# Optimization experiments

Measured on AMD Instinct MI355X. Metric: run time of the kernel, lower is better.

## Reference

```python
import jax, jax.numpy as jnp
import numpy as np

K_NN = 3
EPS = 1e-8
MASK_THRESH = 0.5


def _three_nn_interpolate(pts, known, feats):
    """pts: (B,N,3), known: (B,M,3), feats: (B,M,C) -> (B,N,C).
    Squared-distance 3-NN + inverse-distance weighted interpolation
    (pointnet2 three_nn / three_interpolate semantics)."""
    # (B,N,M) squared euclidean distances
    d2 = (jnp.sum(pts * pts, -1)[:, :, None]
          + jnp.sum(known * known, -1)[:, None, :]
          - 2.0 * jnp.einsum('bnd,bmd->bnm', pts, known))
    neg_d, idx = jax.lax.top_k(-d2, K_NN)          # (B,N,3)
    dist = jnp.maximum(-neg_d, 0.0)                # squared dists, clamp fp error
    dist_recip = 1.0 / (dist + EPS)
    weight = dist_recip / jnp.sum(dist_recip, -1, keepdims=True)  # (B,N,3)
    b_idx = jnp.arange(pts.shape[0])[:, None, None]
    gathered = feats[b_idx, idx]                   # (B,N,3,C)
    return jnp.sum(weight[..., None] * gathered, axis=2)  # (B,N,C)


def setup_inputs() -> dict:
    key = jax.random.key(0)
    ks = jax.random.split(key, 10)
    B, N, C = 4, 8192, 32
    M2, M3, M4, Mm = 8192, 4096, 2048, 4096
    sc = 10.0  # spread coords over a realistic metric range
    return {
        'points_mean': jax.random.normal(ks[0], (B, N, 3)) * sc,
        'known2': jax.random.normal(ks[1], (B, M2, 3)) * sc,
        'feats2': jax.random.normal(ks[2], (B, M2, C)),
        'known3': jax.random.normal(ks[3], (B, M3, 3)) * sc,
        'feats3': jax.random.normal(ks[4], (B, M3, C)),
        'known4': jax.random.normal(ks[5], (B, M4, 3)) * sc,
        'feats4': jax.random.normal(ks[6], (B, M4, C)),
        'match_points': jax.random.normal(ks[7], (B, Mm, 3)) * sc,
        'w_fc': jax.random.normal(ks[8], (64, 96)) * 0.1,
        'w_cls': jax.random.normal(ks[9], (1, 64)) * 0.1,
    }


def reference(points_mean, known2, feats2, known3, feats3, known4, feats4,
              match_points, w_fc, w_cls):
    p0 = _three_nn_interpolate(points_mean, known2, feats2)  # (B,N,32)
    p1 = _three_nn_interpolate(points_mean, known3, feats3)
    p2 = _three_nn_interpolate(points_mean, known4, feats4)
    pointwise = jnp.concatenate([p0, p1, p2], axis=-1) @ w_fc.T  # (B,N,64)
    pred_hm = pointwise @ w_cls.T                                 # (B,N,1)
    # GT mask: min distance to match points < 0.5 m
    d2 = (jnp.sum(points_mean * points_mean, -1)[:, :, None]
          + jnp.sum(match_points * match_points, -1)[:, None, :]
          - 2.0 * jnp.einsum('bnd,bmd->bnm', points_mean, match_points))
    min_d = jnp.sqrt(jnp.maximum(jnp.min(d2, axis=-1), 0.0))      # (B,N)
    gt_hm = (min_d < MASK_THRESH).astype(jnp.float32)
    return pred_hm, gt_hm
```

## Files before the change

### kernel.cpp

```cpp
#include <hip/hip_runtime.h>

typedef unsigned int u32;
typedef unsigned long long u64;
typedef float f32x2 __attribute__((ext_vector_type(2)));

#define NB 4
#define NQ 8192
#define MARGIN 0.0625f
#define NBKT 4096

#define OFF_C0   0u
#define OFF_C1   524288u
#define OFF_C2   786432u
#define OFF_CMP  917504u
#define OFF_SKEY 1179648u
#define OFF_BOX  2031616u
#define WS_NEW2  2068480u
#define OFF_CM   917504u
#define WS_OLD   (512u*1024 + 256u*1024 + 128u*1024 + 512u*1024)

struct __align__(32) CP { f32x2 x, y, z, w; };
struct DM { double x, y, z, w; };

__device__ __forceinline__ f32x2 fma2(f32x2 a, f32x2 b, f32x2 c) {
  return __builtin_elementwise_fma(a, b, c);
}

__device__ __forceinline__ void lexins(double& e0d, double& e1d, double& e2d,
                                       int& e0i, int& e1i, int& e2i,
                                       double d, int i) {
  if (d < e2d || (d == e2d && i < e2i)) {
    if (d < e0d || (d == e0d && i < e0i)) {
      e2d = e1d; e2i = e1i; e1d = e0d; e1i = e0i; e0d = d; e0i = i;
    } else if (d < e1d || (d == e1d && i < e1i)) {
      e2d = e1d; e2i = e1i; e1d = d; e1i = i;
    } else {
      e2d = d; e2i = i;
    }
  }
}

__device__ __forceinline__ void ins4(float kv, u32 idx,
                                     float& k0, float& k1, float& k2, float& k3,
                                     u32& i0, u32& i1, u32& i2, u32& i3) {
  if (kv < k3) {
    bool lt0 = kv < k0, lt1 = kv < k1, lt2 = kv < k2;
    k3 = lt2 ? k2 : kv;               i3 = lt2 ? i2 : idx;
    k2 = lt2 ? (lt1 ? k1 : kv) : k2;  i2 = lt2 ? (lt1 ? i1 : idx) : i2;
    k1 = lt1 ? (lt0 ? k0 : kv) : k1;  i1 = lt1 ? (lt0 ? i0 : idx) : i1;
    k0 = lt0 ? kv : k0;               i0 = lt0 ? idx : i0;
  }
}

__device__ __forceinline__ u32 spread10(u32 v) {
  v &= 0x3FFu;
  v = (v | (v << 16)) & 0x030000FFu;
  v = (v | (v << 8))  & 0x0300F00Fu;
  v = (v | (v << 4))  & 0x030C30C3u;
  v = (v | (v << 2))  & 0x09249249u;
  return v;
}
__device__ __forceinline__ u32 morton30(float x, float y, float z) {
  int xi = (int)((x + 64.f) * 8.f);
  int yi = (int)((y + 64.f) * 8.f);
  int zi = (int)((z + 64.f) * 8.f);
  xi = min(max(xi, 0), 1023); yi = min(max(yi, 0), 1023); zi = min(max(zi, 0), 1023);
  return spread10((u32)xi) | (spread10((u32)yi) << 1) | (spread10((u32)zi) << 2);
}

__device__ __forceinline__ size_t skey_abase(int arr) {
  return (arr == 0) ? 0 : (arr == 1) ? 32768 : (arr == 2) ? 49152
        : (arr == 3) ? 57344 : 73728;
}

__global__ __launch_bounds__(1024) void prep_csort(
    const float* __restrict__ k2p, const float* __restrict__ k3p,
    const float* __restrict__ k4p, const float* __restrict__ mmp,
    const float* __restrict__ pts, u64* __restrict__ skey) {
  __shared__ u32 hist[NBKT];
  const int arr = blockIdx.x, b = blockIdx.y, tid = threadIdx.x;
  const float* src = (arr == 0) ? k2p : (arr == 1) ? k3p : (arr == 2) ? k4p
                      : (arr == 3) ? mmp : pts;
  const int n = (arr == 0) ? 8192 : (arr == 1) ? 4096 : (arr == 2) ? 2048
                 : (arr == 3) ? 4096 : 8192;
  const float* sb = src + (size_t)b * n * 3;
  u64* skb = skey + skey_abase(arr) + (size_t)b * n;

  for (int i = tid; i < NBKT; i += 1024) hist[i] = 0;
  __syncthreads();
  for (int i = tid; i < n; i += 1024) {
    u32 k = morton30(sb[3 * i], sb[3 * i + 1], sb[3 * i + 2]);
    atomicAdd(&hist[k >> 18], 1u);
  }
  __syncthreads();
  for (int d = 1; d < NBKT; d <<= 1) {
    for (int i = tid; i < NBKT / (2 * d); i += 1024) {
      int idx = (2 * i + 2) * d - 1;
      hist[idx] += hist[idx - d];
    }
    __syncthreads();
  }
  if (tid == 0) hist[NBKT - 1] = 0;
  __syncthreads();
  for (int d = NBKT >> 1; d >= 1; d >>= 1) {
    for (int i = tid; i < NBKT / (2 * d); i += 1024) {
      int idx = (2 * i + 2) * d - 1;
      u32 t = hist[idx - d];
      hist[idx - d] = hist[idx];
      hist[idx] += t;
    }
    __syncthreads();
  }
  for (int i = tid; i < n; i += 1024) {
    u32 k = morton30(sb[3 * i], sb[3 * i + 1], sb[3 * i + 2]);
    u32 pos = atomicAdd(&hist[k >> 18], 1u);
    skb[pos] = ((u64)k << 32) | (u32)i;
  }
}

__global__ __launch_bounds__(512) void refine_emit(
    const float* __restrict__ k2p, const float* __restrict__ k3p,
    const float* __restrict__ k4p, const float* __restrict__ mmp,
    const float* __restrict__ pts, u64* __restrict__ skey,
    CP* __restrict__ c0, CP* __restrict__ c1, CP* __restrict__ c2,
    CP* __restrict__ cmp, float* __restrict__ boxes) {
  __shared__ u64 ex[512];
  const int widx = blockIdx.x, b = blockIdx.y, tid = threadIdx.x;
  int arr, win;
  if (widx < 16)      { arr = 0; win = widx; }
  else if (widx < 24) { arr = 1; win = widx - 16; }
  else if (widx < 28) { arr = 2; win = widx - 24; }
  else if (widx < 36) { arr = 3; win = widx - 28; }
  else                { arr = 4; win = widx - 36; }
  const float* src = (arr == 0) ? k2p : (arr == 1) ? k3p : (arr == 2) ? k4p
                      : (arr == 3) ? mmp : pts;
  const int n = (arr == 0) ? 8192 : (arr == 1) ? 4096 : (arr == 2) ? 2048
                 : (arr == 3) ? 4096 : 8192;
  u64* skb = skey + skey_abase(arr) + (size_t)b * n;
  const int e = win * 512 + tid;
  u64 v = skb[e];

  for (int k = 2; k <= 512; k <<= 1) {
    for (int j = k >> 1; j > 0; j >>= 1) {
      u64 w;
      if (j < 64) {
        w = __shfl_xor(v, j);
      } else {
        __syncthreads();
        ex[tid] = v;
        __syncthreads();
        w = ex[tid ^ j];
      }
      bool up = (tid & k) == 0;
      bool lower = (tid & j) == 0;
      v = (up == lower) ? (v < w ? v : w) : (v < w ? w : v);
    }
  }
  skb[e] = v;
  if (arr == 4) return;

  u32 p = (u32)v;
  const float* sb = src + (size_t)b * n * 3;
  float x = sb[3 * p], y = sb[3 * p + 1], z = sb[3 * p + 2];
  {
    CP* dst = (arr == 0) ? c0 : (arr == 1) ? c1 : (arr == 2) ? c2 : cmp;
    float* df = (float*)(dst + (size_t)b * (n >> 1) + (e >> 1));
    int sl = e & 1;
    df[sl]     = x;
    df[2 + sl] = y;
    df[4 + sl] = z;
    df[6 + sl] = fmaf(z, z, fmaf(y, y, x * x));
  }
  float xlo = x, xhi = x, ylo = y, yhi = y, zlo = z, zhi = z;
#pragma unroll
  for (int off = 1; off < 64; off <<= 1) {
    xlo = fminf(xlo, __shfl_xor(xlo, off)); xhi = fmaxf(xhi, __shfl_xor(xhi, off));
    ylo = fminf(ylo, __shfl_xor(ylo, off)); yhi = fmaxf(yhi, __shfl_xor(yhi, off));
    zlo = fminf(zlo, __shfl_xor(zlo, off)); zhi = fmaxf(zhi, __shfl_xor(zhi, off));
  }
  if ((tid & 63) == 0) {
    const int nG = n >> 6, g = e >> 6;
    const int boff = (arr == 0) ? 0 : (arr == 1) ? 512 : (arr == 2) ? 768 : 896;
    float* bx = boxes + ((size_t)boff + (size_t)b * nG + g) * 8;
    bx[0] = xlo; bx[1] = xhi; bx[2] = ylo; bx[3] = yhi; bx[4] = zlo; bx[5] = zhi;
    bx[6] = 0.f; bx[7] = 0.f;
  }
}

__device__ __forceinline__ void scan_pairs16(
    const CP* __restrict__ cg, u32 ebase,
    f32x2 mx2, f32x2 my2, f32x2 mz2,
    float& k0, float& k1, float& k2, float& k3,
    u32& i0, u32& i1, u32& i2, u32& i3) {
#pragma unroll 4
  for (int gg = 0; gg < 16; gg += 4) {
    f32x2 key[4];
#pragma unroll
    for (int u = 0; u < 4; ++u) {
      CP c = cg[gg + u];
      key[u] = fma2(mx2, c.x, fma2(my2, c.y, fma2(mz2, c.z, c.w)));
    }
#pragma unroll
    for (int u = 0; u < 4; ++u) {
      float ka = key[u].x, kb = key[u].y;
      if (fminf(ka, kb) < k3) {
        u32 ib = ebase + (u32)((gg + u) * 2);
        ins4(ka, ib,     k0, k1, k2, k3, i0, i1, i2, i3);
        ins4(kb, ib + 1, k0, k1, k2, k3, i0, i1, i2, i3);
      }
    }
  }
}

struct Smem4 {
  float  box[2304];
  float  qx[32], qy[32], qz[32];
  double qdx[32], qdy[32], qdz[32], qn[32];
  u32    oq[32];
  u32    di[3][32][4][4];
  double mmin[32][8];
  float  wv[96];
  float  wq[32][9];
  u32    iq[32][9];
  float  contrib[32][9];
  float4 stage[4][2][64];
  u32    list[4][64];
};

__global__ __launch_bounds__(256, 4) void fused_sorted3(
    const float* __restrict__ pts,
    const float* __restrict__ f2, const float* __restrict__ f3,
    const float* __restrict__ f4,
    const float* __restrict__ wfc, const float* __restrict__ wcls,
    const CP* __restrict__ c0, const CP* __restrict__ c1,
    const CP* __restrict__ c2, const CP* __restrict__ cmp,
    const u64* __restrict__ skey, const float* __restrict__ boxes,
    float* __restrict__ out) {
  __shared__ Smem4 s;
  const int tid = threadIdx.x;
  const int b = blockIdx.y;
  const int tile = blockIdx.x;
  const int lane = tid & 63;
  const int q = tid & 31;
  const int h = (tid >> 5) & 1;
  const int wid = __builtin_amdgcn_readfirstlane(tid >> 6);

  for (int i = tid; i < 2304; i += 256) {
    int src;
    if (i < 1024)      src = (b * 128) * 8 + i;
    else if (i < 1536) src = (512 + b * 64) * 8 + (i - 1024);
    else if (i < 1792) src = (768 + b * 32) * 8 + (i - 1536);
    else               src = (896 + b * 64) * 8 + (i - 1792);
    s.box[i] = boxes[src];
  }
  if (tid < 32) {
    u64 kv = skey[73728 + (size_t)b * NQ + tile * 32 + tid];
    u32 p = (u32)kv;
    const float* pb = pts + (size_t)b * NQ * 3;
    float x = pb[3 * p], y = pb[3 * p + 1], z = pb[3 * p + 2];
    s.qx[tid] = x; s.qy[tid] = y; s.qz[tid] = z; s.oq[tid] = p;
    double dx = (double)x, dy = (double)y, dz = (double)z;
    s.qdx[tid] = dx; s.qdy[tid] = dy; s.qdz[tid] = dz;
    s.qn[tid] = (dx * dx + dy * dy) + dz * dz;
  } else if (tid < 128) {
    int t = tid - 32;
    float acc = 0.f;
    for (int j = 0; j < 64; ++j) acc += wcls[j] * wfc[j * 96 + t];
    s.wv[t] = acc;
  }
  __syncthreads();

  const float qx = s.qx[q], qy = s.qy[q], qz = s.qz[q];
  const float qnf = fmaf(qz, qz, fmaf(qy, qy, qx * qx));
  const float fm2x = -2.0f * qx, fm2y = -2.0f * qy, fm2z = -2.0f * qz;
  const double qdx = s.qdx[q], qdy = s.qdy[q], qdz = s.qdz[q], qn = s.qn[q];
  const f32x2 mx2 = {fm2x, fm2x}, my2 = {fm2y, fm2y}, mz2 = {fm2z, fm2z};

  {
    int lvl, part, nG, g0, stride, nvote, lboff;
    if (wid < 2)      { lvl = 0; nG = 128; stride = 2; nvote = 63;
                        g0 = (((tile * 128) >> 8) & ~1) | wid;
                        part = wid * 2 + h; lboff = 0; }
    else if (wid == 2){ lvl = 1; nG = 64;  stride = 1; nvote = 63;
                        g0 = (tile * 64) >> 8; part = h; lboff = 128; }
    else              { lvl = 2; nG = 32;  stride = 1; nvote = 31;
                        g0 = (tile * 32) >> 8; part = h; lboff = 192; }
    const int M = 8192 >> lvl;
    const CP* c4 = ((lvl == 0) ? c0 : ((lvl == 1) ? c1 : c2)) + (((size_t)b * M) >> 1);

    float k0 = __builtin_inff(), k1 = k0, k2 = k0, k3 = k0;
    u32 i0 = 0, i1 = 0, i2 = 0, i3 = 0;

    scan_pairs16(c4 + g0 * 32 + h * 16, (u32)(g0 * 64 + h * 32),
                 mx2, my2, mz2, k0, k1, k2, k3, i0, i1, i2, i3);

    int nl = 0;
    for (int t = 1; t <= nvote; ++t) {
      int g = (g0 + stride * t) & (nG - 1);
      const float* bx = &s.box[(lboff + g) * 8];
      float dx = fmaxf(fmaxf(bx[0] - qx, qx - bx[1]), 0.f);
      float dy = fmaxf(fmaxf(bx[2] - qy, qy - bx[3]), 0.f);
      float dz = fmaxf(fmaxf(bx[4] - qz, qz - bx[5]), 0.f);
      float lb = fmaf(dx, dx, fmaf(dy, dy, dz * dz));
      if (__any(lb < qnf + k3 + MARGIN)) {
        if (lane == 0) s.list[wid][nl] = (u32)g;
        ++nl;
      }
    }

    auto accept = [&](int g) -> bool {
      const float* bx = &s.box[(lboff + g) * 8];
      float dx = fmaxf(fmaxf(bx[0] - qx, qx - bx[1]), 0.f);
      float dy = fmaxf(fmaxf(bx[2] - qy, qy - bx[3]), 0.f);
      float dz = fmaxf(fmaxf(bx[4] - qz, qz - bx[5]), 0.f);
      float lb = fmaf(dx, dx, fmaf(dy, dy, dz * dz));
      return __any(lb < qnf + k3 + MARGIN);
    };
    int ip = 0, cur = 0, gcur = -1;
    float4 v;
    while (ip < nl) {
      int g = (int)s.list[wid][ip++];
      if (accept(g)) { gcur = g; v = ((const float4*)(c4 + (size_t)g * 32))[lane]; break; }
    }
    while (gcur >= 0) {
      s.stage[wid][cur][lane] = v;
      int gn = -1;
      while (ip < nl) {
        int g = (int)s.list[wid][ip++];
        if (accept(g)) { gn = g; break; }
      }
      if (gn >= 0) v = ((const float4*)(c4 + (size_t)gn * 32))[lane];
      const CP* sg = (const CP*)&s.stage[wid][cur][0];
      scan_pairs16(sg + h * 16, (u32)(gcur * 64 + h * 32),
                   mx2, my2, mz2, k0, k1, k2, k3, i0, i1, i2, i3);
      gcur = gn; cur ^= 1;
    }

    s.di[lvl][q][part][0] = i0; s.di[lvl][q][part][1] = i1;
    s.di[lvl][q][part][2] = i2; s.di[lvl][q][part][3] = i3;
  }

  {
    const CP* cmb = cmp + (size_t)b * 2048;
    int gm0 = tile >> 2;
    double dmin = __builtin_inf();
    for (int t = 0; t < 16; ++t) {
      int g = (gm0 + wid + 4 * t) & 63;
      const float* bx = &s.box[(224 + g) * 8];
      float dx = fmaxf(fmaxf(bx[0] - qx, qx - bx[1]), 0.f);
      float dy = fmaxf(fmaxf(bx[2] - qy, qy - bx[3]), 0.f);
      float dz = fmaxf(fmaxf(bx[4] - qz, qz - bx[5]), 0.f);
      float lb = fmaf(dx, dx, fmaf(dy, dy, dz * dz));
      if (__any(lb < 0.26f)) {
        const CP* cg = cmb + g * 32 + h * 16;
#pragma unroll 4
        for (int p = 0; p < 16; ++p) {
          CP c = cg[p];
          f32x2 key = fma2(mx2, c.x, fma2(my2, c.y, fma2(mz2, c.z, c.w)));
          if (fminf(key.x, key.y) + qnf < 0.252f) {
            {
              double x = (double)c.x.x, y = (double)c.y.x, z = (double)c.z.x;
              double kn2 = (x * x + y * y) + z * z;
              double dot = (qdx * x + qdy * y) + qdz * z;
              dmin = fmin(dmin, (qn + kn2) - 2.0 * dot);
            }
            {
              double x = (double)c.x.y, y = (double)c.y.y, z = (double)c.z.y;
              double kn2 = (x * x + y * y) + z * z;
              double dot = (qdx * x + qdy * y) + qdz * z;
              dmin = fmin(dmin, (qn + kn2) - 2.0 * dot);
            }
          }
        }
      }
    }
    s.mmin[q][wid * 2 + h] = dmin;
  }
  __syncthreads();

  const int gqbase = b * NQ;
  if (tid < 96) {
    const int lvl = tid >> 5;
    const int qq = tid & 31;
    const int M  = 8192 >> lvl;
    const int np = (lvl == 0) ? 4 : 2;
    const CP* c4 = ((lvl == 0) ? c0 : ((lvl == 1) ? c1 : c2)) + (((size_t)b * M) >> 1);
    const u64* skl = skey + ((lvl == 0) ? 0 : (lvl == 1) ? 32768 : 49152)
                     + (size_t)b * M;
    const double tqdx = s.qdx[qq], tqdy = s.qdy[qq], tqdz = s.qdz[qq], tqn = s.qn[qq];
    double e0 = __builtin_inf(), e1 = e0, e2 = e0;
    int j0 = 0, j1 = 0, j2 = 0;
    for (int hh = 0; hh < np; ++hh) {
#pragma unroll
      for (int r = 0; r < 4; ++r) {
        int sidx = (int)s.di[lvl][qq][hh][r];
        CP cc = c4[sidx >> 1];
        bool hi = sidx & 1;
        double x = (double)(hi ? cc.x.y : cc.x.x);
        double y = (double)(hi ? cc.y.y : cc.y.x);
        double z = (double)(hi ? cc.z.y : cc.z.x);
        int orig = (int)(u32)skl[sidx];
        double kn2 = (x * x + y * y) + z * z;
        double dot = (tqdx * x + tqdy * y) + tqdz * z;
        double d2 = (tqn + kn2) - 2.0 * dot;
        lexins(e0, e1, e2, j0, j1, j2, d2, orig);
      }
    }
    double d0 = fmax(e0, 0.0), d1 = fmax(e1, 0.0), d2v = fmax(e2, 0.0);
    double r0 = 1.0 / (d0 + 1e-8);
    double r1 = 1.0 / (d1 + 1e-8);
    double r2 = 1.0 / (d2v + 1e-8);
    double sum = (r0 + r1) + r2;
    s.wq[qq][lvl * 3 + 0] = (float)(r0 / sum); s.iq[qq][lvl * 3 + 0] = (u32)j0;
    s.wq[qq][lvl * 3 + 1] = (float)(r1 / sum); s.iq[qq][lvl * 3 + 1] = (u32)j1;
    s.wq[qq][lvl * 3 + 2] = (float)(r2 / sum); s.iq[qq][lvl * 3 + 2] = (u32)j2;
  } else if (tid < 128) {
    const int qq = tid - 96;
    double dm = s.mmin[qq][0];
#pragma unroll
    for (int p = 1; p < 8; ++p) dm = fmin(dm, s.mmin[qq][p]);
    out[NB * NQ + gqbase + (int)s.oq[qq]] = (dm < 0.25) ? 1.0f : 0.0f;
  }
  __syncthreads();

  for (int item = tid; item < 288; item += 256) {
    const int qq = item & 31, j = item >> 5;
    const int lvl = j / 3;
    const float* fp = (lvl == 0) ? f2 : ((lvl == 1) ? f3 : f4);
    const int M = 8192 >> lvl;
    const float4* row = (const float4*)(fp + ((size_t)b * M + s.iq[qq][j]) * 32);
    const float* wvp = s.wv + lvl * 32;
    float acc = 0.f;
#pragma unroll
    for (int v = 0; v < 8; ++v) {
      float4 r = row[v];
      acc += wvp[4 * v] * r.x + wvp[4 * v + 1] * r.y
           + wvp[4 * v + 2] * r.z + wvp[4 * v + 3] * r.w;
    }
    s.contrib[qq][j] = s.wq[qq][j] * acc;
  }
  __syncthreads();
  if (tid < 32) {
    const float* c = s.contrib[tid];
    float l0 = (c[0] + c[1]) + c[2];
    float l1 = (c[3] + c[4]) + c[5];
    float l2 = (c[6] + c[7]) + c[8];
    out[gqbase + (int)s.oq[tid]] = (l0 + l1) + l2;
  }
}

__global__ __launch_bounds__(256) void prep_kernel(
    const float* __restrict__ k2p, const float* __restrict__ k3p,
    const float* __restrict__ k4p, const float* __restrict__ mmp,
    CP* __restrict__ c0, CP* __restrict__ c1,
    CP* __restrict__ c2, DM* __restrict__ cm) {
  int r = blockIdx.y;
  int i = blockIdx.x * 256 + threadIdx.x;
  if (r < 3) {
    const float* src = (r == 0) ? k2p : ((r == 1) ? k3p : k4p);
    CP* dst = (r == 0) ? c0 : ((r == 1) ? c1 : c2);
    int pairs = (r == 0) ? NB * 4096 : ((r == 1) ? NB * 2048 : NB * 1024);
    if (i >= pairs) return;
    const float* p = src + (size_t)i * 6;
    float x0 = p[0], y0 = p[1], z0 = p[2];
    float x1 = p[3], y1 = p[4], z1 = p[5];
    CP c;
    c.x = f32x2{x0, x1}; c.y = f32x2{y0, y1}; c.z = f32x2{z0, z1};
    c.w = f32x2{fmaf(z0, z0, fmaf(y0, y0, x0 * x0)),
                fmaf(z1, z1, fmaf(y1, y1, x1 * x1))};
    dst[i] = c;
  } else {
    if (i >= NB * 4096) return;
    double x = (double)mmp[3 * i], y = (double)mmp[3 * i + 1], z = (double)mmp[3 * i + 2];
    DM d = {x, y, z, fma(z, z, fma(y, y, x * x))};
    cm[i] = d;
  }
}

template <bool PREP>
__device__ __forceinline__ void scan_nn(
    const CP* __restrict__ cp, const float* __restrict__ raw,
    int gstart, int L, float m2x, float m2y, float m2z,
    float* kk, u32* ii) {
  float k0 = __builtin_inff(), k1 = k0, k2 = k0, k3 = k0;
  u32 i0 = 0, i1 = 0, i2 = 0, i3 = 0;
  if (PREP) {
    const f32x2 mx2 = {m2x, m2x}, my2 = {m2y, m2y}, mz2 = {m2z, m2z};
    const int G = L >> 1;
#pragma unroll 2
    for (int g = 0; g < G; g += 4) {
      f32x2 key[4];
#pragma unroll
      for (int u = 0; u < 4; ++u) {
        CP c = cp[g + u];
        key[u] = fma2(mx2, c.x, fma2(my2, c.y, fma2(mz2, c.z, c.w)));
      }
#pragma unroll
      for (int u = 0; u < 4; ++u) {
        float ka = key[u].x, kb = key[u].y;
        if (fminf(ka, kb) < k3) {
          u32 ib = (u32)(gstart + 2 * (g + u));
          ins4(ka, ib,     k0, k1, k2, k3, i0, i1, i2, i3);
          ins4(kb, ib + 1, k0, k1, k2, k3, i0, i1, i2, i3);
        }
      }
    }
  } else {
    for (int j = 0; j < L; j += 8) {
      float key[8];
#pragma unroll
      for (int u = 0; u < 8; ++u) {
        const float* p = raw + (size_t)(gstart + j + u) * 3;
        float x = p[0], y = p[1], z = p[2];
        float n2 = fmaf(z, z, fmaf(y, y, x * x));
        key[u] = fmaf(m2x, x, fmaf(m2y, y, fmaf(m2z, z, n2)));
      }
#pragma unroll
      for (int u = 0; u < 8; ++u)
        ins4(key[u], (u32)(gstart + j + u), k0, k1, k2, k3, i0, i1, i2, i3);
    }
  }
  kk[0] = k0; kk[1] = k1; kk[2] = k2; kk[3] = k3;
  ii[0] = i0; ii[1] = i1; ii[2] = i2; ii[3] = i3;
}

template <bool PREP>
__device__ __forceinline__ double scan_mask(
    const DM* __restrict__ c8, const float* __restrict__ raw,
    int gstart, int L, double m2x, double m2y, double m2z) {
  double smin = __builtin_inf();
  if (PREP) {
    for (int j = 0; j < L; j += 8) {
      double sv[8];
#pragma unroll
      for (int u = 0; u < 8; ++u) {
        DM c = c8[gstart + j + u];
        sv[u] = fma(m2x, c.x, fma(m2y, c.y, fma(m2z, c.z, c.w)));
      }
      double m01 = fmin(sv[0], sv[1]), m23 = fmin(sv[2], sv[3]);
      double m45 = fmin(sv[4], sv[5]), m67 = fmin(sv[6], sv[7]);
      smin = fmin(smin, fmin(fmin(m01, m23), fmin(m45, m67)));
    }
  } else {
    for (int j = 0; j < L; j += 4) {
#pragma unroll
      for (int u = 0; u < 4; ++u) {
        const float* p = raw + (size_t)(gstart + j + u) * 3;
        double x = (double)p[0], y = (double)p[1], z = (double)p[2];
        double kn = fma(z, z, fma(y, y, x * x));
        smin = fmin(smin, fma(m2x, x, fma(m2y, y, fma(m2z, z, kn))));
      }
    }
  }
  return smin;
}

struct Smem {
  float  qx[64], qy[64], qz[64];
  double qdx[64], qdy[64], qdz[64], qn[64];
  float  dk[3][64][4][4];
  u32    di[3][64][4][4];
  double mmin[64][8];
  float  wv[96];
  float  part[64][3];
};

template <bool PREP>
__global__ __launch_bounds__(512, 2) void fused_kernel(
    const float* __restrict__ pts,
    const float* __restrict__ k2p, const float* __restrict__ f2,
    const float* __restrict__ k3p, const float* __restrict__ f3,
    const float* __restrict__ k4p, const float* __restrict__ f4,
    const float* __restrict__ mmp,
    const float* __restrict__ wfc, const float* __restrict__ wcls,
    const CP* __restrict__ c0, const CP* __restrict__ c1,
    const CP* __restrict__ c2, const DM* __restrict__ cm,
    float* __restrict__ out) {
  __shared__ Smem s;
  const int tid = threadIdx.x;
  const int b = blockIdx.y;
  const int q0 = blockIdx.x * 64;
  const int qloc = tid & 63;
  const int wid = __builtin_amdgcn_readfirstlane(tid >> 6);

  if (tid < 64) {
    int gq = b * NQ + q0 + tid;
    float x = pts[3 * gq], y = pts[3 * gq + 1], z = pts[3 * gq + 2];
    s.qx[tid] = x; s.qy[tid] = y; s.qz[tid] = z;
    double dx = (double)x, dy = (double)y, dz = (double)z;
    s.qdx[tid] = dx; s.qdy[tid] = dy; s.qdz[tid] = dz;
    s.qn[tid] = (dx * dx + dy * dy) + dz * dz;
  } else if (tid < 160) {
    int t = tid - 64;
    float acc = 0.f;
    for (int j = 0; j < 64; ++j) acc += wcls[j] * wfc[j * 96 + t];
    s.wv[t] = acc;
  }
  __syncthreads();

  const float fm2x = -2.0f * s.qx[qloc];
  const float fm2y = -2.0f * s.qy[qloc];
  const float fm2z = -2.0f * s.qz[qloc];
  const double dm2x = -2.0 * s.qdx[qloc];
  const double dm2y = -2.0 * s.qdy[qloc];
  const double dm2z = -2.0 * s.qdz[qloc];

  {
    int lvl, prt, gstart, glen;
    if (wid < 4)      { lvl = 0; prt = wid;     gstart = wid * 2048;       glen = 2048; }
    else if (wid < 6) { lvl = 1; prt = wid - 4; gstart = (wid - 4) * 2048; glen = 2048; }
    else              { lvl = 2; prt = wid - 6; gstart = (wid - 6) * 1024; glen = 1024; }
    const CP* c4 = (lvl == 0) ? c0 : ((lvl == 1) ? c1 : c2);
    const float* raw = (lvl == 0) ? k2p : ((lvl == 1) ? k3p : k4p);
    const int      M = (lvl == 0) ? 8192 : ((lvl == 1) ? 4096 : 2048);
    float kk[4]; u32 ii[4];
    scan_nn<PREP>(c4 + (PREP ? (((size_t)b * M + gstart) >> 1) : 0),
                  raw + (size_t)b * M * 3,
                  gstart, glen, fm2x, fm2y, fm2z, kk, ii);
#pragma unroll
    for (int r = 0; r < 4; ++r) {
      s.dk[lvl][qloc][prt][r] = kk[r];
      s.di[lvl][qloc][prt][r] = ii[r];
    }
    int mstart, mlen;
    if (wid < 6) { mstart = wid * 256; mlen = 256; }
    else         { mstart = 1536 + (wid - 6) * 1280; mlen = 1280; }
    s.mmin[qloc][wid] = scan_mask<PREP>(cm + (PREP ? (size_t)b * 4096 : 0),
                                        mmp + (size_t)b * 4096 * 3,
                                        mstart, mlen, dm2x, dm2y, dm2z);
  }
  __syncthreads();

  const int gqbase = b * NQ + q0;
  if (tid < 192) {
    const int lvl = __builtin_amdgcn_readfirstlane(tid >> 6);
    const int q = tid & 63;
    const float* kp = (lvl == 0) ? k2p : ((lvl == 1) ? k3p : k4p);
    const int    M  = (lvl == 0) ? 8192 : ((lvl == 1) ? 4096 : 2048);
    const int    np = (lvl == 0) ? 4 : 2;
    const double qdx = s.qdx[q], qdy = s.qdy[q], qdz = s.qdz[q], qn = s.qn[q];
    double e0 = __builtin_inf(), e1 = e0, e2 = e0;
    int i0 = 0, i1 = 0, i2 = 0;
    for (int h = 0; h < np; ++h) {
#pragma unroll
      for (int r = 0; r < 4; ++r) {
        int idx = (int)s.di[lvl][q][h][r];
        const float* c = kp + ((size_t)b * M + idx) * 3;
        double x = (double)c[0], y = (double)c[1], z = (double)c[2];
        double kn2 = (x * x + y * y) + z * z;
        double dot = (qdx * x + qdy * y) + qdz * z;
        double d2 = (qn + kn2) - 2.0 * dot;
        lexins(e0, e1, e2, i0, i1, i2, d2, idx);
      }
    }
    double d0 = fmax(e0, 0.0), d1 = fmax(e1, 0.0), d2v = fmax(e2, 0.0);
    double r0 = 1.0 / (d0 + 1e-8);
    double r1 = 1.0 / (d1 + 1e-8);
    double r2 = 1.0 / (d2v + 1e-8);
    double sum = (r0 + r1) + r2;
    float wa = (float)(r0 / sum), wb = (float)(r1 / sum), wc = (float)(r2 / sum);
    const float* fp = (lvl == 0) ? f2 : ((lvl == 1) ? f3 : f4);
    const float* g0 = fp + ((size_t)b * M + i0) * 32;
    const float* g1 = fp + ((size_t)b * M + i1) * 32;
    const float* g2 = fp + ((size_t)b * M + i2) * 32;
    float acc = 0.f;
#pragma unroll
    for (int wd = 0; wd < 32; ++wd) {
      float v = (wa * g0[wd] + wb * g1[wd]) + wc * g2[wd];
      acc += s.wv[lvl * 32 + wd] * v;
    }
    s.part[q][lvl] = acc;
  } else if (tid < 256) {
    const int q = tid - 192;
    double sm = s.mmin[q][0];
#pragma unroll
    for (int p = 1; p < 8; ++p) sm = fmin(sm, s.mmin[q][p]);
    double dm = s.qn[q] + sm;
    out[NB * NQ + gqbase + q] = (dm < 0.25) ? 1.0f : 0.0f;
  }
  __syncthreads();
  if (tid < 64) {
    float pred = (s.part[tid][0] + s.part[tid][1]) + s.part[tid][2];
    out[gqbase + tid] = pred;
  }
}

extern "C" void kernel_launch(void* const* d_in, const int* in_sizes, int n_in,
                              void* d_out, int out_size, void* d_ws, size_t ws_size,
                              hipStream_t stream) {
  const float* pts    = (const float*)d_in[0];
  const float* known2 = (const float*)d_in[1];
  const float* feats2 = (const float*)d_in[2];
  const float* known3 = (const float*)d_in[3];
  const float* feats3 = (const float*)d_in[4];
  const float* known4 = (const float*)d_in[5];
  const float* feats4 = (const float*)d_in[6];
  const float* match  = (const float*)d_in[7];
  const float* wfc    = (const float*)d_in[8];
  const float* wcls   = (const float*)d_in[9];

  char* ws = (char*)d_ws;
  CP* c0 = (CP*)(ws + OFF_C0);
  CP* c1 = (CP*)(ws + OFF_C1);
  CP* c2 = (CP*)(ws + OFF_C2);

  if (ws_size >= WS_NEW2) {
    CP* cmp = (CP*)(ws + OFF_CMP);
    u64* skey = (u64*)(ws + OFF_SKEY);
    float* boxes = (float*)(ws + OFF_BOX);
    hipLaunchKernelGGL(prep_csort, dim3(5, NB), dim3(1024), 0, stream,
                       known2, known3, known4, match, pts, skey);
    hipLaunchKernelGGL(refine_emit, dim3(52, NB), dim3(512), 0, stream,
                       known2, known3, known4, match, pts, skey,
                       c0, c1, c2, cmp, boxes);
    hipLaunchKernelGGL(fused_sorted3, dim3(NQ / 32, NB), dim3(256), 0, stream,
                       pts, feats2, feats3, feats4, wfc, wcls,
                       c0, c1, c2, cmp, skey, boxes, (float*)d_out);
  } else if (ws_size >= WS_OLD) {
    DM* cm = (DM*)(ws + OFF_CM);
    hipLaunchKernelGGL(prep_kernel, dim3(64, 4), dim3(256), 0, stream,
                       known2, known3, known4, match, c0, c1, c2, cm);
    hipLaunchKernelGGL(HIP_KERNEL_NAME(fused_kernel<true>), dim3(NQ / 64, NB),
                       dim3(512), 0, stream, pts, known2, feats2, known3, feats3,
                       known4, feats4, match, wfc, wcls, c0, c1, c2, cm,
                       (float*)d_out);
  } else {
    DM* cm = (DM*)(ws + OFF_CM);
    hipLaunchKernelGGL(HIP_KERNEL_NAME(fused_kernel<false>), dim3(NQ / 64, NB),
                       dim3(512), 0, stream, pts, known2, feats2, known3, feats3,
                       known4, feats4, match, wfc, wcls, c0, c1, c2, cm,
                       (float*)d_out);
  }
}
```

Before: 229.9 us.

## Sort candidate groups by tile-box lower bound and prune with wave-wide bound

Replaces the per-query box voting over a fixed group order with one lower bound per group, computed against the bounding box of the wave's queries, with one group per lane. Groups are bitonic-sorted by that bound through wave shuffles and scanned nearest-first, stopping once the next bound exceeds the wave-maximum current k3 bound. The shared-memory box copy and candidate list are removed, and the match-point pass now uses a ballot over per-lane box tests. This trades the looser tile-wide bound and the sorting cost for earlier termination and less shared memory and per-query box work.

Result: slower. 276.3 us (+20.2%).

```diff
diff --git a/kernel.cpp b/kernel.cpp
--- a/kernel.cpp
+++ b/kernel.cpp
@@ -24,6 +24,17 @@
 
 __device__ __forceinline__ f32x2 fma2(f32x2 a, f32x2 b, f32x2 c) {
   return __builtin_elementwise_fma(a, b, c);
+}
+
+__device__ __forceinline__ float wmaxf(float v) {
+#pragma unroll
+  for (int o = 32; o; o >>= 1) v = fmaxf(v, __shfl_xor(v, o));
+  return v;
+}
+__device__ __forceinline__ float wminf(float v) {
+#pragma unroll
+  for (int o = 32; o; o >>= 1) v = fminf(v, __shfl_xor(v, o));
+  return v;
 }
 
 __device__ __forceinline__ void lexins(double& e0d, double& e1d, double& e2d,
@@ -212,8 +223,7 @@
   }
 }
 
-struct Smem4 {
-  float  box[2304];
+struct Smem5 {
   float  qx[32], qy[32], qz[32];
   double qdx[32], qdy[32], qdz[32], qn[32];
   u32    oq[32];
@@ -224,10 +234,9 @@
   u32    iq[32][9];
   float  contrib[32][9];
   float4 stage[4][2][64];
-  u32    list[4][64];
 };
 
-__global__ __launch_bounds__(256, 4) void fused_sorted3(
+__global__ __launch_bounds__(256, 4) void fused_sorted4(
     const float* __restrict__ pts,
     const float* __restrict__ f2, const float* __restrict__ f3,
     const float* __restrict__ f4,
@@ -236,7 +245,7 @@
     const CP* __restrict__ c2, const CP* __restrict__ cmp,
     const u64* __restrict__ skey, const float* __restrict__ boxes,
     float* __restrict__ out) {
-  __shared__ Smem4 s;
+  __shared__ Smem5 s;
   const int tid = threadIdx.x;
   const int b = blockIdx.y;
   const int tile = blockIdx.x;
@@ -245,14 +254,6 @@
   const int h = (tid >> 5) & 1;
   const int wid = __builtin_amdgcn_readfirstlane(tid >> 6);
 
-  for (int i = tid; i < 2304; i += 256) {
-    int src;
-    if (i < 1024)      src = (b * 128) * 8 + i;
-    else if (i < 1536) src = (512 + b * 64) * 8 + (i - 1024);
-    else if (i < 1792) src = (768 + b * 32) * 8 + (i - 1536);
-    else               src = (896 + b * 64) * 8 + (i - 1792);
-    s.box[i] = boxes[src];
-  }
   if (tid < 32) {
     u64 kv = skey[73728 + (size_t)b * NQ + tile * 32 + tid];
     u32 p = (u32)kv;
@@ -276,63 +277,72 @@
   const double qdx = s.qdx[q], qdy = s.qdy[q], qdz = s.qdz[q], qn = s.qn[q];
   const f32x2 mx2 = {fm2x, fm2x}, my2 = {fm2y, fm2y}, mz2 = {fm2z, fm2z};
 
+  const float txlo = wminf(qx), txhi = wmaxf(qx);
+  const float tylo = wminf(qy), tyhi = wmaxf(qy);
+  const float tzlo = wminf(qz), tzhi = wmaxf(qz);
+
+  auto boxS = [&](const float* bxb, int gl) -> float {
+    const float4* bp = (const float4*)(bxb + (size_t)gl * 8);
+    float4 blo = bp[0], bhi = bp[1];
+    float dx = fmaxf(fmaxf(blo.x - txhi, txlo - blo.y), 0.f);
+    float dy = fmaxf(fmaxf(blo.z - tyhi, tylo - blo.w), 0.f);
+    float dz = fmaxf(fmaxf(bhi.x - tzhi, tzlo - bhi.y), 0.f);
+    return fmaf(dx, dx, fmaf(dy, dy, dz * dz));
+  };
+
   {
-    int lvl, part, nG, g0, stride, nvote, lboff;
-    if (wid < 2)      { lvl = 0; nG = 128; stride = 2; nvote = 63;
-                        g0 = (((tile * 128) >> 8) & ~1) | wid;
-                        part = wid * 2 + h; lboff = 0; }
-    else if (wid == 2){ lvl = 1; nG = 64;  stride = 1; nvote = 63;
-                        g0 = (tile * 64) >> 8; part = h; lboff = 128; }
-    else              { lvl = 2; nG = 32;  stride = 1; nvote = 31;
-                        g0 = (tile * 32) >> 8; part = h; lboff = 192; }
+    int lvl, part, gl;
+    bool valid = true;
+    if (wid < 2)      { lvl = 0; part = wid * 2 + h; gl = wid + 2 * lane; }
+    else if (wid == 2){ lvl = 1; part = h;           gl = lane; }
+    else              { lvl = 2; part = h;           gl = lane & 31; valid = lane < 32; }
     const int M = 8192 >> lvl;
+    const int nG = M >> 6;
     const CP* c4 = ((lvl == 0) ? c0 : ((lvl == 1) ? c1 : c2)) + (((size_t)b * M) >> 1);
+    const float* bxb = boxes +
+        (size_t)(((lvl == 0) ? 0 : ((lvl == 1) ? 512 : 768)) + b * nG) * 8;
+
+    float Ss = valid ? boxS(bxb, gl) : __builtin_inff();
+    u32 gs = (u32)gl;
+#pragma unroll
+    for (int k = 2; k <= 64; k <<= 1) {
+#pragma unroll
+      for (int j = k >> 1; j > 0; j >>= 1) {
+        float So = __shfl_xor(Ss, j);
+        u32  go = __shfl_xor(gs, j);
+        bool up = ((lane & k) == 0) == ((lane & j) == 0);
+        bool take = up ? (So < Ss) : (So > Ss);
+        if (take) { Ss = So; gs = go; }
+      }
+    }
 
     float k0 = __builtin_inff(), k1 = k0, k2 = k0, k3 = k0;
     u32 i0 = 0, i1 = 0, i2 = 0, i3 = 0;
-
-    scan_pairs16(c4 + g0 * 32 + h * 16, (u32)(g0 * 64 + h * 32),
-                 mx2, my2, mz2, k0, k1, k2, k3, i0, i1, i2, i3);
-
-    int nl = 0;
-    for (int t = 1; t <= nvote; ++t) {
-      int g = (g0 + stride * t) & (nG - 1);
-      const float* bx = &s.box[(lboff + g) * 8];
-      float dx = fmaxf(fmaxf(bx[0] - qx, qx - bx[1]), 0.f);
-      float dy = fmaxf(fmaxf(bx[2] - qy, qy - bx[3]), 0.f);
-      float dz = fmaxf(fmaxf(bx[4] - qz, qz - bx[5]), 0.f);
-      float lb = fmaf(dx, dx, fmaf(dy, dy, dz * dz));
-      if (__any(lb < qnf + k3 + MARGIN)) {
-        if (lane == 0) s.list[wid][nl] = (u32)g;
-        ++nl;
-      }
-    }
-
-    auto accept = [&](int g) -> bool {
-      const float* bx = &s.box[(lboff + g) * 8];
-      float dx = fmaxf(fmaxf(bx[0] - qx, qx - bx[1]), 0.f);
-      float dy = fmaxf(fmaxf(bx[2] - qy, qy - bx[3]), 0.f);
-      float dz = fmaxf(fmaxf(bx[4] - qz, qz - bx[5]), 0.f);
-      float lb = fmaf(dx, dx, fmaf(dy, dy, dz * dz));
-      return __any(lb < qnf + k3 + MARGIN);
-    };
-    int ip = 0, cur = 0, gcur = -1;
+    float Bmax = __builtin_inff();
+
+    int i = 1, cur = 0, gcur = -1;
     float4 v;
-    while (ip < nl) {
-      int g = (int)s.list[wid][ip++];
-      if (accept(g)) { gcur = g; v = ((const float4*)(c4 + (size_t)g * 32))[lane]; break; }
+    {
+      float S0 = __shfl(Ss, 0);
+      if (S0 < Bmax) { gcur = (int)__shfl(gs, 0);
+                       v = ((const float4*)(c4 + (size_t)gcur * 32))[lane]; }
     }
     while (gcur >= 0) {
       s.stage[wid][cur][lane] = v;
       int gn = -1;
-      while (ip < nl) {
-        int g = (int)s.list[wid][ip++];
-        if (accept(g)) { gn = g; break; }
-      }
-      if (gn >= 0) v = ((const float4*)(c4 + (size_t)gn * 32))[lane];
+      if (i < 64) {
+        float Sn = __shfl(Ss, i);
+        if (Sn < Bmax) { gn = (int)__shfl(gs, i);
+                         v = ((const float4*)(c4 + (size_t)gn * 32))[lane]; ++i; }
+      }
       const CP* sg = (const CP*)&s.stage[wid][cur][0];
       scan_pairs16(sg + h * 16, (u32)(gcur * 64 + h * 32),
                    mx2, my2, mz2, k0, k1, k2, k3, i0, i1, i2, i3);
+      Bmax = wmaxf(qnf + k3) + MARGIN;
+      if (gn >= 0) {
+        float Sg = __shfl(Ss, i - 1);
+        if (Sg >= Bmax) gn = -1;
+      }
       gcur = gn; cur ^= 1;
     }
 
@@ -342,34 +352,31 @@
 
   {
     const CP* cmb = cmp + (size_t)b * 2048;
-    int gm0 = tile >> 2;
+    const float* bxb = boxes + (size_t)(896 + b * 64) * 8;
+    int glm = wid + 4 * (lane & 15);
+    float Sm = (lane < 16) ? boxS(bxb, glm) : __builtin_inff();
+    u64 bal = __ballot(Sm < 0.26f);
     double dmin = __builtin_inf();
-    for (int t = 0; t < 16; ++t) {
-      int g = (gm0 + wid + 4 * t) & 63;
-      const float* bx = &s.box[(224 + g) * 8];
-      float dx = fmaxf(fmaxf(bx[0] - qx, qx - bx[1]), 0.f);
-      float dy = fmaxf(fmaxf(bx[2] - qy, qy - bx[3]), 0.f);
-      float dz = fmaxf(fmaxf(bx[4] - qz, qz - bx[5]), 0.f);
-      float lb = fmaf(dx, dx, fmaf(dy, dy, dz * dz));
-      if (__any(lb < 0.26f)) {
-        const CP* cg = cmb + g * 32 + h * 16;
+    while (bal) {
+      int bp = __builtin_ctzll(bal); bal &= bal - 1;
+      int g = __shfl(glm, bp);
+      const CP* cg = cmb + g * 32 + h * 16;
 #pragma unroll 4
-        for (int p = 0; p < 16; ++p) {
-          CP c = cg[p];
-          f32x2 key = fma2(mx2, c.x, fma2(my2, c.y, fma2(mz2, c.z, c.w)));
-          if (fminf(key.x, key.y) + qnf < 0.252f) {
-            {
-              double x = (double)c.x.x, y = (double)c.y.x, z = (double)c.z.x;
-              double kn2 = (x * x + y * y) + z * z;
-              double dot = (qdx * x + qdy * y) + qdz * z;
-              dmin = fmin(dmin, (qn + kn2) - 2.0 * dot);
-            }
-            {
-              double x = (double)c.x.y, y = (double)c.y.y, z = (double)c.z.y;
-              double kn2 = (x * x + y * y) + z * z;
-              double dot = (qdx * x + qdy * y) + qdz * z;
-              dmin = fmin(dmin, (qn + kn2) - 2.0 * dot);
-            }
+      for (int p = 0; p < 16; ++p) {
+        CP c = cg[p];
+        f32x2 key = fma2(mx2, c.x, fma2(my2, c.y, fma2(mz2, c.z, c.w)));
+        if (fminf(key.x, key.y) + qnf < 0.252f) {
+          {
+            double x = (double)c.x.x, y = (double)c.y.x, z = (double)c.z.x;
+            double kn2 = (x * x + y * y) + z * z;
+            double dot = (qdx * x + qdy * y) + qdz * z;
+            dmin = fmin(dmin, (qn + kn2) - 2.0 * dot);
+          }
+          {
+            double x = (double)c.x.y, y = (double)c.y.y, z = (double)c.z.y;
+            double kn2 = (x * x + y * y) + z * z;
+            double dot = (qdx * x + qdy * y) + qdz * z;
+            dmin = fmin(dmin, (qn + kn2) - 2.0 * dot);
           }
         }
       }
@@ -713,7 +720,7 @@
     hipLaunchKernelGGL(refine_emit, dim3(52, NB), dim3(512), 0, stream,
                        known2, known3, known4, match, pts, skey,
                        c0, c1, c2, cmp, boxes);
-    hipLaunchKernelGGL(fused_sorted3, dim3(NQ / 32, NB), dim3(256), 0, stream,
+    hipLaunchKernelGGL(fused_sorted4, dim3(NQ / 32, NB), dim3(256), 0, stream,
                        pts, feats2, feats3, feats4, wfc, wcls,
                        c0, c1, c2, cmp, skey, boxes, (float*)d_out);
   } else if (ws_size >= WS_OLD) {
```
